# Optimization experiments

Hardware: AMD Instinct MI355X
Metric: run time of the kernel (lower is better)

The kernel has to match this reference:

```python
import jax, jax.numpy as jnp
import numpy as np

EPS = float(np.finfo(np.float32).eps)
B, N, NUM_ATOM, K = 16, 256, 64, 20
NUM_EDGETYPE = 3
SHORT = (1, 2, 3)
LONG = (3, 5, 7)
HIDDEN = (128, 128)
OUT = 1
SCALES = len(SHORT) + len(LONG) + NUM_EDGETYPE + 1  # 10
LB = 1e-4  # lanczos breakdown tolerance


def _xavier(k, fi, fo):
    return jax.random.uniform(k, (fi, fo), jnp.float32, -1.0, 1.0) * (6.0 / (fi + fo)) ** 0.5


def setup_inputs() -> dict:
    key = jax.random.key(0)
    ks = jax.random.split(key, 12)
    inp = {}
    inp["node_feat"] = jax.random.randint(ks[0], (B, N), 0, NUM_ATOM)
    inp["L"] = jax.random.uniform(ks[1], (B, N, N, NUM_EDGETYPE + 1), jnp.float32)
    # embedding_map: Linear(num_atom,1024) -> ReLU -> Linear(1024,num_atom)
    inp["emb_w1"] = _xavier(ks[2], NUM_ATOM, 1024); inp["emb_b1"] = jnp.zeros((1024,), jnp.float32)
    inp["emb_w2"] = _xavier(ks[3], 1024, NUM_ATOM); inp["emb_b2"] = jnp.zeros((NUM_ATOM,), jnp.float32)
    # eigen_map per long scale: Linear(K*K,1024) -> ReLU -> Linear(1024,K*K)
    S, K2 = len(LONG), K * K
    inp["eig_w1"] = jnp.stack([_xavier(jax.random.fold_in(ks[4], i), K2, 1024) for i in range(S)])
    inp["eig_b1"] = jnp.zeros((S, 1024), jnp.float32)
    inp["eig_w2"] = jnp.stack([_xavier(jax.random.fold_in(ks[5], i), 1024, K2) for i in range(S)])
    inp["eig_b2"] = jnp.zeros((S, K2), jnp.float32)
    dims = [NUM_ATOM] + list(HIDDEN) + [OUT]
    inp["filt_w0"] = _xavier(ks[6], dims[0] * SCALES, dims[1]); inp["filt_b0"] = jnp.zeros((dims[1],), jnp.float32)
    inp["filt_w1"] = _xavier(ks[7], dims[1] * SCALES, dims[2]); inp["filt_b1"] = jnp.zeros((dims[2],), jnp.float32)
    inp["filt_wo"] = _xavier(ks[8], dims[2], dims[3]); inp["filt_bo"] = jnp.zeros((dims[3],), jnp.float32)
    inp["att_w"] = _xavier(ks[9], dims[2], 1); inp["att_b"] = jnp.zeros((1,), jnp.float32)
    return inp


def _graph_laplacian(feat, adj_mask):
    # feat: B x N x D; pairwise gaussian affinity, sym-normalized (alpha=0.5)
    diff = feat[:, :, None, :] - feat[:, None, :, :]           # B,N,N,D
    dist2 = jnp.sum(diff * diff, axis=-1).reshape(B, -1)       # B,N*N
    sigma2 = jnp.mean(dist2, axis=1, keepdims=True)
    A = jnp.exp(-dist2 / sigma2).reshape(B, N, N) * adj_mask
    row_sum = jnp.sum(A, axis=2, keepdims=True)
    pad = jnp.where(row_sum == 0.0, 1.0, 0.0)
    D = 1.0 / jnp.sqrt(row_sum + pad)
    return D * A * jnp.swapaxes(D, 1, 2)


def _lanczos(A, key):
    # sequential Lanczos tridiagonalization with double Gram-Schmidt reorth
    q = jax.random.normal(key, (B, N), jnp.float32)
    q = q / jnp.linalg.norm(q, axis=1, keepdims=True)

    def step(carry, i):
        Qbuf, q_prev, qc, beta_prev, valid = carry
        z = jnp.einsum('bij,bj->bi', A, qc)
        alpha = jnp.sum(qc * z, axis=1)
        z = z - alpha[:, None] * qc - beta_prev[:, None] * q_prev
        for _ in range(2):  # reorthogonalize against Q[1..ii-1] (zero cols are no-ops)
            coef = jnp.einsum('bnk,bn->bk', Qbuf, z) / (jnp.sum(Qbuf * Qbuf, axis=1) + EPS)
            z = z - jnp.einsum('bnk,bk->bn', Qbuf, coef)
        beta = jnp.sqrt(jnp.sum(z * z, axis=1))
        valid = valid * (beta >= LB).astype(jnp.float32)
        q_next = z * valid[:, None] / (beta[:, None] + EPS)
        Qbuf = Qbuf.at[:, :, i].set(qc)
        return (Qbuf, qc, q_next, beta, valid), (alpha, beta, valid, qc)

    init = (jnp.zeros((B, N, K), jnp.float32), jnp.zeros((B, N), jnp.float32), q,
            jnp.zeros((B,), jnp.float32), jnp.ones((B,), jnp.float32))
    _, (alphas, betas, valids, qs) = jax.lax.scan(step, init, jnp.arange(K))
    alpha = alphas.T            # B,K
    beta = betas.T              # B,K
    valid = valids.T            # B,K (cumulative 1..1 0..0)
    idx = jnp.sum(valid, axis=1).astype(jnp.int32)   # rank per sample
    alpha = alpha * valid
    beta = beta[:, :K - 1] * valid[:, :K - 1]
    T = jax.vmap(lambda a, b: jnp.diag(a) + jnp.diag(b, 1) + jnp.diag(b, -1))(alpha, beta)
    Q = jnp.transpose(qs, (1, 2, 0))  # B,N,K
    # faithful to source: zero node rows >= idx_mask (only when idx < N)
    row_ok = (jnp.arange(N)[None, :] < idx[:, None]) | (idx[:, None] >= N)
    Q = Q * valid[:, None, :] * row_ok[:, :, None].astype(jnp.float32)
    return T, Q


def _spectral_filters(T, Q, eig_w1, eig_b1, eig_w2, eig_b2, key):
    T_list = []
    TT = T
    b = jax.random.normal(key, (B, K, 1), jnp.float32)
    Tb = b / jnp.linalg.norm(b, axis=1, keepdims=True)
    for ii in range(max(LONG) + 1):
        if ii in LONG:
            T_list.append(TT)
        TT = TT @ T
        # power-iteration cap on spectral radius
        Tb_new = T @ Tb
        l_max = jnp.sum(Tb_new * Tb, axis=1, keepdims=True) / (jnp.sum(Tb * Tb, axis=1, keepdims=True) + EPS)
        TT = TT * (jnp.abs(l_max) <= 1.0).astype(jnp.float32)
        Tb = Tb_new / (jnp.linalg.norm(Tb_new, axis=1, keepdims=True) + EPS)
    triu = jnp.triu(jnp.ones((K, K), jnp.float32))
    eye = jnp.eye(K, dtype=jnp.float32)
    outs = []
    for s in range(len(LONG)):
        h = jax.nn.relu(T_list[s].reshape(B, -1) @ eig_w1[s] + eig_b1[s])
        DD = (h @ eig_w2[s] + eig_b2[s]).reshape(B, K, K)
        DD = DD * triu
        DD = DD + jnp.swapaxes(DD, 1, 2) * (1.0 - eye)  # symmetrize
        outs.append(jnp.einsum('bnk,bkl,bml->bnm', Q, DD, Q))
    return jnp.stack(outs, axis=3)  # B,N,N,S


def reference(node_feat, L, emb_w1, emb_b1, emb_w2, emb_b2, eig_w1, eig_b1, eig_w2, eig_b2,
              filt_w0, filt_b0, filt_w1, filt_b1, filt_wo, filt_bo, att_w, att_b):
    key = jax.random.key(42)
    state = jax.nn.one_hot(node_feat, NUM_ATOM, dtype=jnp.float32)  # frozen identity embedding
    feat = jax.nn.relu(state @ emb_w1 + emb_b1) @ emb_w2 + emb_b2
    Lk = _graph_laplacian(feat, L[:, :, :, 0])
    T, Q = _lanczos(Lk, jax.random.fold_in(key, 0))
    filt_w = (filt_w0, filt_w1)
    filt_b = (filt_b0, filt_b1)
    for tt in range(len(HIDDEN)):
        msg = []
        DD = _spectral_filters(T, Q, eig_w1, eig_b1, eig_w2, eig_b2, jax.random.fold_in(key, tt + 1))
        tmp = state
        for ii in range(1, max(SHORT) + 1):  # short diffusion
            tmp = jnp.einsum('bij,bjd->bid', Lk, tmp)
            if ii in SHORT:
                msg.append(tmp)
        for s in range(len(LONG)):           # long (spectral) diffusion
            msg.append(jnp.einsum('bij,bjd->bid', DD[:, :, :, s], state))
        for e in range(NUM_EDGETYPE + 1):     # per-edgetype propagation
            msg.append(jnp.einsum('bij,bjd->bid', L[:, :, :, e], state))
        msg = jnp.concatenate(msg, axis=2)    # B,N,10*D
        state = jax.nn.relu(msg @ filt_w[tt] + filt_b[tt])
    y = state @ filt_wo + filt_bo             # B,N,1
    att = jax.nn.sigmoid(state @ att_w + att_b)
    score = jnp.mean(att * y, axis=1)          # B,OUT (mask=None -> mean over nodes)
    return score
```

## Files before the change

kernel.cpp:

```cpp
#include <hip/hip_runtime.h>


constexpr int nB = 16;
constexpr int nN = 256;
constexpr int nK = 20;
constexpr int QS = nN + 1;
constexpr float EPSF = 1.1920928955078125e-07f;
constexpr float LBF  = 1e-4f;

#define DEV static __device__ __forceinline__

DEV void tf2x32(unsigned k0, unsigned k1, unsigned x0, unsigned x1,
                unsigned &o0, unsigned &o1) {
  unsigned ks2 = k0 ^ k1 ^ 0x1BD11BDAu;
#define RND(r) { x0 += x1; x1 = (x1 << r) | (x1 >> (32 - r)); x1 ^= x0; }
  x0 += k0;  x1 += k1;
  RND(13) RND(15) RND(26) RND(6)
  x0 += k1;  x1 += ks2 + 1u;
  RND(17) RND(29) RND(16) RND(24)
  x0 += ks2; x1 += k0 + 2u;
  RND(13) RND(15) RND(26) RND(6)
  x0 += k0;  x1 += k1 + 3u;
  RND(17) RND(29) RND(16) RND(24)
  x0 += k1;  x1 += ks2 + 4u;
  RND(13) RND(15) RND(26) RND(6)
  x0 += ks2; x1 += k0 + 5u;
#undef RND
  o0 = x0; o1 = x1;
}

DEV float erfinv_f32(float x) {
  float w = -log1pf(-x * x);
  float p;
  if (w < 5.0f) {
    w -= 2.5f;
    p = 2.81022636e-08f;
    p = fmaf(p, w, 3.43273939e-07f);
    p = fmaf(p, w, -3.5233877e-06f);
    p = fmaf(p, w, -4.39150654e-06f);
    p = fmaf(p, w, 0.00021858087f);
    p = fmaf(p, w, -0.00125372503f);
    p = fmaf(p, w, -0.00417768164f);
    p = fmaf(p, w, 0.246640727f);
    p = fmaf(p, w, 1.50140941f);
  } else {
    w = sqrtf(w) - 3.0f;
    p = -0.000200214257f;
    p = fmaf(p, w, 0.000100950558f);
    p = fmaf(p, w, 0.00134934322f);
    p = fmaf(p, w, -0.00367342844f);
    p = fmaf(p, w, 0.00573950773f);
    p = fmaf(p, w, -0.0076224613f);
    p = fmaf(p, w, 0.00943887047f);
    p = fmaf(p, w, 1.00167406f);
    p = fmaf(p, w, 2.83297682f);
  }
  return p * x;
}

DEV float jax_normal(unsigned k0, unsigned k1, unsigned idx) {
  unsigned o0, o1;
  tf2x32(k0, k1, 0u , idx , o0, o1);
  unsigned bits = o0 ^ o1;
  float u = __uint_as_float((bits >> 9) | 0x3f800000u) - 1.0f;
  const float lo = -0.99999994f;
  float v = fmaxf(lo, u * 2.0f + lo);
  return 1.41421356237309515f * erfinv_f32(v);
}

DEV double waveRedD(double v) {
#pragma unroll
  for (int m = 32; m > 0; m >>= 1) v += __shfl_xor(v, m, 64);
  return v;
}
DEV float waveRedF(float v) {
#pragma unroll
  for (int m = 32; m > 0; m >>= 1) v += __shfl_xor(v, m, 64);
  return v;
}
DEV double blockSumD(double v, double *s4) {
  v = waveRedD(v);
  int w = threadIdx.x >> 6;
  __syncthreads();
  if ((threadIdx.x & 63) == 0) s4[w] = v;
  __syncthreads();
  return s4[0] + s4[1] + s4[2] + s4[3];
}
DEV double sum8(const double *r) {
  return ((r[0] + r[1]) + (r[2] + r[3])) + ((r[4] + r[5]) + (r[6] + r[7]));
}

__global__ __launch_bounds__(256) void feat_table_kernel(
    const float *__restrict__ w1, const float *__restrict__ b1,
    const float *__restrict__ w2, const float *__restrict__ b2,
    float *__restrict__ table) {
  int a = blockIdx.x, t = threadIdx.x;
  __shared__ float hh[1024];
  __shared__ float part[256];
  for (int k = t; k < 1024; k += 256)
    hh[k] = fmaxf(w1[(size_t)a * 1024 + k] + b1[k], 0.f);
  __syncthreads();
  int d = t & 63, slice = t >> 6;
  float acc = 0.f;
  for (int k = slice * 256; k < slice * 256 + 256; k++)
    acc += hh[k] * w2[(size_t)k * 64 + d];
  part[t] = acc;
  __syncthreads();
  if (t < 64)
    table[(size_t)a * 64 + t] =
        part[t] + part[64 + t] + part[128 + t] + part[192 + t] + b2[t];
}

__global__ __launch_bounds__(256) void feat_state_tr_kernel(
    const int *__restrict__ nf, const float *__restrict__ table,
    float *__restrict__ feat, float *__restrict__ featT,
    float *__restrict__ state0) {
  int g = blockIdx.x;
  int bb = g >> 2, n0 = (g & 3) * 64;
  int t = threadIdx.x;
  int c = t & 63, r4 = t >> 6;
  __shared__ float tl[64][65];
  __shared__ int av[64];
  if (t < 64) av[t] = nf[bb * nN + n0 + t];
  __syncthreads();
  for (int r = r4; r < 64; r += 4) {
    int a = av[r];
    float v = table[(size_t)a * 64 + c];
    tl[r][c] = v;
    feat[((size_t)(bb * nN + n0 + r)) * 64 + c] = v;
    state0[((size_t)(bb * nN + n0 + r)) * 64 + c] = (c == a) ? 1.f : 0.f;
  }
  __syncthreads();
  for (int r = r4; r < 64; r += 4)
    featT[(size_t)bb * 16384 + (size_t)r * nN + n0 + c] = tl[c][r];
}

__global__ __launch_bounds__(256) void dist2_kernel(
    const float *__restrict__ feat, const float *__restrict__ featT,
    float *__restrict__ G, double *__restrict__ part) {
  int g = blockIdx.x;
  int bb = g >> 6, i0 = (g & 63) * 4;
  int t = threadIdx.x;
  __shared__ float fi[4][64];
  __shared__ double s4[4];
  {
    int r = t >> 6, d = t & 63;
    fi[r][d] = feat[((size_t)(bb * nN + i0 + r)) * 64 + d];
  }
  __syncthreads();
  const float *ft = featT + (size_t)bb * 16384 + t;
  float a0 = 0.f, a1 = 0.f, a2 = 0.f, a3 = 0.f;
#pragma unroll 8
  for (int d = 0; d < 64; d++) {
    float x = ft[(size_t)d * nN];
    float d0 = fi[0][d] - x; a0 += d0 * d0;
    float d1 = fi[1][d] - x; a1 += d1 * d1;
    float d2 = fi[2][d] - x; a2 += d2 * d2;
    float d3 = fi[3][d] - x; a3 += d3 * d3;
  }
  size_t base = ((size_t)bb * nN + i0) * nN + t;
  G[base]           = a0;
  G[base + nN]      = a1;
  G[base + 2 * nN]  = a2;
  G[base + 3 * nN]  = a3;
  double tot = blockSumD((double)a0 + (double)a1 + (double)a2 + (double)a3, s4);
  if (t == 0) part[g] = tot;
}

__global__ __launch_bounds__(64) void sigred_kernel(
    const double *__restrict__ part, float *__restrict__ sigma2) {
  int bb = blockIdx.x, t = threadIdx.x;
  double v = part[(size_t)bb * 64 + t];
  v = waveRedD(v);
  if (t == 0) sigma2[bb] = (float)(v / 65536.0);
}

__global__ __launch_bounds__(256) void arow_kernel(
    const float *__restrict__ Lfull, const float *__restrict__ sigma2,
    float *__restrict__ G, float *__restrict__ Dv) {
  int g = blockIdx.x;
  int i = g % nN, bb = g / nN;
  int t = threadIdx.x;
  __shared__ double s4[4];
  float sig = sigma2[bb];
  size_t idx2 = ((size_t)bb * nN + i) * nN + t;
  float a = expf(-G[idx2] / sig) * Lfull[idx2 * 4];
  G[idx2] = a;
  double rs = blockSumD((double)a, s4);
  if (t == 0) {
    float r = (float)rs;
    float pad = (r == 0.f) ? 1.f : 0.f;
    Dv[(size_t)bb * nN + i] = 1.f / sqrtf(r + pad);
  }
}

__global__ __launch_bounds__(256) void lkscale_tr_kernel(
    float *__restrict__ G, const float *__restrict__ Dv,
    float *__restrict__ GT) {
  int g = blockIdx.x;
  int bb = g >> 4, tile = g & 15;
  int ti = (tile >> 2) * 64, tj = (tile & 3) * 64;
  int t = threadIdx.x;
  int lj = t & 63, li0 = t >> 6;
  __shared__ float tl[64][65];
  for (int r = li0; r < 64; r += 4) {
    int i = ti + r;
    size_t idx = ((size_t)bb * nN + i) * nN + tj + lj;
    float v = Dv[(size_t)bb * nN + i] * G[idx] * Dv[(size_t)bb * nN + tj + lj];
    G[idx] = v;
    tl[r][lj] = v;
  }
  __syncthreads();
  for (int r = li0; r < 64; r += 4) {
    int j = tj + r;
    GT[((size_t)bb * nN + j) * nN + ti + lj] = tl[lj][r];
  }
}

__global__ __launch_bounds__(512)
void lanczos_kernel(const float *__restrict__ GT, float *__restrict__ Qout,
                    float *__restrict__ Tout) {
  __shared__ float Qb[nK * QS];
  __shared__ float qc[nN], qp[nN], zz[nN];
  __shared__ double zp[2][nN];
  __shared__ float qn2[nK], sAl[nK], sBe[nK], sVa[nK], coef[nK];
  __shared__ double redA[8], redB[8];
  int bb = blockIdx.x, u = threadIdx.x;
  int t = u & 255, h = u >> 8;
  int wv = u >> 6, lane = u & 63;
  int gid = u >> 4, gl = u & 15;

  const float *Gcol = GT + (size_t)bb * (nN * nN) + (size_t)(h * 128) * nN + t;

  unsigned k0, k1;
  tf2x32(0u, 42u, 0u, 0u, k0, k1);
  float val = 0.f;
  if (h == 0) val = jax_normal(k0, k1, (unsigned)(bb * nN + t));
  {
    double v = waveRedD((double)val * (double)val);
    __syncthreads();
    if (lane == 0) redA[wv] = v;
    __syncthreads();
    double n2 = sum8(redA);
    if (h == 0) {
      qc[t] = val / sqrtf((float)n2);
      qp[t] = 0.f;
    }
  }
  __syncthreads();

  float beta_prev = 0.f, validf = 1.f;

  for (int i = 0; i < nK; i++) {
    double a0 = 0, a1 = 0, a2 = 0, a3 = 0, a4 = 0, a5 = 0, a6 = 0, a7 = 0;
    {
      const float *qv = qc + h * 128;
#pragma unroll
      for (int jj = 0; jj < 128; jj += 8) {
        a0 += (double)Gcol[(size_t)(jj + 0) * nN] * (double)qv[jj + 0];
        a1 += (double)Gcol[(size_t)(jj + 1) * nN] * (double)qv[jj + 1];
        a2 += (double)Gcol[(size_t)(jj + 2) * nN] * (double)qv[jj + 2];
        a3 += (double)Gcol[(size_t)(jj + 3) * nN] * (double)qv[jj + 3];
        a4 += (double)Gcol[(size_t)(jj + 4) * nN] * (double)qv[jj + 4];
        a5 += (double)Gcol[(size_t)(jj + 5) * nN] * (double)qv[jj + 5];
        a6 += (double)Gcol[(size_t)(jj + 6) * nN] * (double)qv[jj + 6];
        a7 += (double)Gcol[(size_t)(jj + 7) * nN] * (double)qv[jj + 7];
      }
    }
    double part = ((a0 + a1) + (a2 + a3)) + ((a4 + a5) + (a6 + a7));
    zp[h][t] = part;
    double apart = (double)qc[t] * part;
    double qpart = (h == 0) ? (double)qc[t] * (double)qc[t] : 0.0;
    apart = waveRedD(apart);
    qpart = waveRedD(qpart);
    if (lane == 0) { redA[wv] = apart; redB[wv] = qpart; }
    __syncthreads();
    float alpha = (float)sum8(redA);
    if (h == 0) {
      float zi = (float)(zp[0][t] + zp[1][t]);
      zi = zi - alpha * qc[t] - beta_prev * qp[t];
      zz[t] = zi;
    } else {
      Qb[i * QS + t] = qc[t];
      if (t == 0) qn2[i] = (float)sum8(redB);
    }
    __syncthreads();
    if (gid < i) {
      double p = 0.0;
#pragma unroll
      for (int j = 0; j < 16; j++) {
        int n0 = gl + 16 * j;
        p += (double)Qb[gid * QS + n0] * (double)zz[n0];
      }
#pragma unroll
      for (int m = 1; m <= 8; m <<= 1) p += __shfl_xor(p, m, 64);
      if (gl == 0)
        coef[gid] = (float)(p / ((double)qn2[gid] + (double)EPSF));
    }
    __syncthreads();
    if (h == 0) {
      double sub = 0.0;
      for (int k = 0; k < i; k++)
        sub += (double)Qb[k * QS + t] * (double)coef[k];
      zz[t] = (float)((double)zz[t] - sub);
    }
    __syncthreads();
    if (gid < i) {
      double p = 0.0;
#pragma unroll
      for (int j = 0; j < 16; j++) {
        int n0 = gl + 16 * j;
        p += (double)Qb[gid * QS + n0] * (double)zz[n0];
      }
#pragma unroll
      for (int m = 1; m <= 8; m <<= 1) p += __shfl_xor(p, m, 64);
      if (gl == 0)
        coef[gid] = (float)(p / ((double)qn2[gid] + (double)EPSF));
    }
    __syncthreads();
    double bpart = 0.0;
    if (h == 0) {
      double sub = 0.0;
      for (int k = 0; k < i; k++)
        sub += (double)Qb[k * QS + t] * (double)coef[k];
      float znew = (float)((double)zz[t] - sub);
      zz[t] = znew;
      bpart = (double)znew * (double)znew;
    }
    bpart = waveRedD(bpart);
    if (lane == 0) redA[wv] = bpart;
    __syncthreads();
    float beta = sqrtf((float)sum8(redA));
    validf *= (beta >= LBF) ? 1.f : 0.f;
    if (u == 0) {
      sAl[i] = alpha;
      sBe[i] = beta;
      sVa[i] = validf;
    }
    if (h == 0) {
      float qnext = zz[t] * validf / (beta + EPSF);
      qp[t] = qc[t];
      qc[t] = qnext;
    }
    __syncthreads();
    beta_prev = beta;
  }

  float idxf = 0.f;
  for (int k = 0; k < nK; k++) idxf += sVa[k];
  int idx = (int)idxf;
  if (h == 0) {
    float rowok = ((t < idx) || (idx >= nN)) ? 1.f : 0.f;
    for (int k = 0; k < nK; k++)
      Qout[((size_t)bb * nN + t) * nK + k] = Qb[k * QS + t] * sVa[k] * rowok;
  }
  for (int e = u; e < nK * nK; e += 512) {
    int i = e / nK, j = e % nK;
    float v = 0.f;
    if (i == j) v = sAl[i] * sVa[i];
    else if (j == i + 1) v = sBe[i] * sVa[i];
    else if (i == j + 1) v = sBe[j] * sVa[j];
    Tout[(size_t)bb * nK * nK + e] = v;
  }
}

__global__ __launch_bounds__(64) void spect_power_kernel(
    const float *__restrict__ Tin, float *__restrict__ Tpow2) {
  __shared__ float T_[nK * nK], TT[nK * nK], TTn[nK * nK];
  __shared__ float Tb[nK], Tbn[nK];
  int bb = blockIdx.x & 15, tt = blockIdx.x >> 4;
  int t = threadIdx.x;
  for (int e = t; e < nK * nK; e += 64) {
    float v = Tin[(size_t)bb * nK * nK + e];
    T_[e] = v;
    TT[e] = v;
  }
  unsigned k0, k1;
  tf2x32(0u, 42u, 0u, (unsigned)(tt + 1), k0, k1);
  if (t < nK) Tb[t] = jax_normal(k0, k1, (unsigned)(bb * nK + t));
  __syncthreads();
  float pv = (t < nK) ? Tb[t] * Tb[t] : 0.f;
  float nb = sqrtf(waveRedF(pv));
  if (t < nK) Tb[t] = Tb[t] / nb;
  __syncthreads();
  for (int ii = 0; ii < 8; ii++) {
    if (ii == 3 || ii == 5 || ii == 7) {
      int s = (ii - 3) / 2;
      int sf = tt * 3 + s;
      for (int e = t; e < nK * nK; e += 64)
        Tpow2[((size_t)sf * nB + bb) * nK * nK + e] = TT[e];
    }
    __syncthreads();
    for (int e = t; e < nK * nK; e += 64) {
      int i = e / nK, j = e % nK;
      float a = 0.f;
      for (int l = 0; l < nK; l++) a += TT[i * nK + l] * T_[l * nK + j];
      TTn[e] = a;
    }
    if (t < nK) {
      float a = 0.f;
      for (int l = 0; l < nK; l++) a += T_[t * nK + l] * Tb[l];
      Tbn[t] = a;
    }
    __syncthreads();
    float pn = (t < nK) ? Tbn[t] * Tb[t] : 0.f;
    float pd = (t < nK) ? Tb[t] * Tb[t] : 0.f;
    float num = waveRedF(pn);
    float den = waveRedF(pd);
    float lmax = num / (den + EPSF);
    float keep = (fabsf(lmax) <= 1.0f) ? 1.f : 0.f;
    __syncthreads();
    for (int e = t; e < nK * nK; e += 64) TT[e] = TTn[e] * keep;
    float p2 = (t < nK) ? Tbn[t] * Tbn[t] : 0.f;
    float nn = sqrtf(waveRedF(p2));
    if (t < nK) Tb[t] = Tbn[t] / (nn + EPSF);
    __syncthreads();
  }
}

__global__ __launch_bounds__(256) void eig1_kernel(
    const float *__restrict__ Tpow2, const float *__restrict__ w1p,
    const float *__restrict__ b1p, float *__restrict__ h2) {
  int g = blockIdx.x;
  int oc = g & 15, sf = g >> 4;
  int sw = sf % 3;
  int t = threadIdx.x;
  int o = (t & 63) + oc * 64, bbg = t >> 6;
  __shared__ float tp[nB * 400];
  for (int e = t; e < nB * 400; e += 256)
    tp[e] = Tpow2[(size_t)sf * nB * 400 + e];
  __syncthreads();
  float bias = b1p[(size_t)sw * 1024 + o];
  float acc0 = bias, acc1 = bias, acc2 = bias, acc3 = bias;
  const float *W = w1p + (size_t)sw * 400 * 1024 + o;
  const float *t0 = tp + (bbg + 0) * 400;
  const float *t1 = tp + (bbg + 4) * 400;
  const float *t2 = tp + (bbg + 8) * 400;
  const float *t3 = tp + (bbg + 12) * 400;
  for (int k = 0; k < 400; k++) {
    float w = W[(size_t)k * 1024];
    acc0 += t0[k] * w;
    acc1 += t1[k] * w;
    acc2 += t2[k] * w;
    acc3 += t3[k] * w;
  }
  h2[((size_t)sf * nB + (bbg + 0))  * 1024 + o] = fmaxf(acc0, 0.f);
  h2[((size_t)sf * nB + (bbg + 4))  * 1024 + o] = fmaxf(acc1, 0.f);
  h2[((size_t)sf * nB + (bbg + 8))  * 1024 + o] = fmaxf(acc2, 0.f);
  h2[((size_t)sf * nB + (bbg + 12)) * 1024 + o] = fmaxf(acc3, 0.f);
}

__global__ __launch_bounds__(256) void eig2_kernel(
    const float *__restrict__ h2, const float *__restrict__ w2p,
    const float *__restrict__ b2p, float *__restrict__ raw2) {
  int g = blockIdx.x;
  int kc = g % 25, sf = g / 25;
  int sw = sf % 3;
  int t = threadIdx.x;
  int kl = (t & 15) + kc * 16, bb = t >> 4;
  __shared__ float hh[nB * 1025];
  for (int e = t; e < nB * 1024; e += 256)
    hh[(e >> 10) * 1025 + (e & 1023)] = h2[(size_t)sf * nB * 1024 + e];
  __syncthreads();
  float acc = b2p[(size_t)sw * 400 + kl];
  const float *W = w2p + (size_t)sw * 1024 * 400 + kl;
  const float *hv = hh + bb * 1025;
  for (int o = 0; o < 1024; o++) acc += hv[o] * W[(size_t)o * 400];
  raw2[((size_t)sf * nB + bb) * 400 + kl] = acc;
}

__global__ void qtstate_kernel(const float *__restrict__ Q,
                               const float *__restrict__ state,
                               float *__restrict__ E) {
  int g = blockIdx.x;
  int k = g % nK, bb = g / nK;
  int t = threadIdx.x, Din = blockDim.x;
  __shared__ float qcol[nN];
  for (int n = t; n < nN; n += Din) qcol[n] = Q[((size_t)bb * nN + n) * nK + k];
  __syncthreads();
  const float *st = state + (size_t)bb * nN * Din;
  float acc = 0.f;
  for (int n = 0; n < nN; n++) acc += qcol[n] * st[(size_t)n * Din + t];
  E[((size_t)bb * nK + k) * Din + t] = acc;
}

__global__ void ddE_kernel(const float *__restrict__ raw,
                           const float *__restrict__ E,
                           float *__restrict__ F) {
  int g = blockIdx.x;
  int k = g % nK, bb = (g / nK) % nB, s = g / (nK * nB);
  int t = threadIdx.x, Din = blockDim.x;
  __shared__ float dr[nK];
  if (t < nK) {
    int mi = k < t ? k : t, ma = k < t ? t : k;
    dr[t] = raw[((size_t)s * nB + bb) * 400 + mi * nK + ma];
  }
  __syncthreads();
  float acc = 0.f;
  for (int l = 0; l < nK; l++)
    acc += dr[l] * E[((size_t)bb * nK + l) * Din + t];
  F[(((size_t)s * nB + bb) * nK + k) * Din + t] = acc;
}

__global__ void lk_matvec_kernel(const float *__restrict__ Lk,
                                 const float *__restrict__ in, int inStride,
                                 float *__restrict__ out, int outStride) {
  int g = blockIdx.x;
  int bb = g >> 5, r0 = (g & 31) * 8;
  int t = threadIdx.x, Din = blockDim.x;
  __shared__ float rows[8][nN];
  for (int e = t; e < 8 * nN; e += Din) {
    int r = e >> 8, j = e & 255;
    rows[r][j] = Lk[((size_t)bb * nN + r0 + r) * nN + j];
  }
  __syncthreads();
  float acc[8] = {0.f, 0.f, 0.f, 0.f, 0.f, 0.f, 0.f, 0.f};
  const float *ip = in + (size_t)bb * nN * inStride + t;
  for (int j = 0; j < nN; j++) {
    float x = ip[(size_t)j * inStride];
#pragma unroll
    for (int r = 0; r < 8; r++) acc[r] += rows[r][j] * x;
  }
#pragma unroll
  for (int r = 0; r < 8; r++)
    out[((size_t)bb * nN + r0 + r) * outStride + t] = acc[r];
}

__global__ void longmsg_kernel(const float *__restrict__ Q,
                               const float *__restrict__ F,
                               float *__restrict__ msg, int C) {
  int g = blockIdx.x;
  int i = g % nN, bb = g / nN;
  int t = threadIdx.x, Din = blockDim.x;
  __shared__ float qr[nK];
  if (t < nK) qr[t] = Q[((size_t)bb * nN + i) * nK + t];
  __syncthreads();
  for (int s = 0; s < 3; s++) {
    float acc = 0.f;
    for (int k = 0; k < nK; k++)
      acc += qr[k] * F[(((size_t)s * nB + bb) * nK + k) * Din + t];
    msg[((size_t)bb * nN + i) * C + (3 + s) * Din + t] = acc;
  }
}

__global__ void edgemsg_kernel(const float *__restrict__ Lfull,
                               const float *__restrict__ state,
                               float *__restrict__ msg, int C) {
  int g = blockIdx.x;
  int bb = g >> 6, r0 = (g & 63) * 4;
  int t = threadIdx.x, Din = blockDim.x;
  __shared__ float4 rows4[4][nN];
  const float4 *L4 = (const float4 *)Lfull;
  for (int e = t; e < 4 * nN; e += Din) {
    int r = e >> 8, j = e & 255;
    rows4[r][j] = L4[((size_t)bb * nN + r0 + r) * nN + j];
  }
  __syncthreads();
  float acc[4][4];
#pragma unroll
  for (int r = 0; r < 4; r++)
#pragma unroll
    for (int e = 0; e < 4; e++) acc[r][e] = 0.f;
  const float *st = state + (size_t)bb * nN * Din + t;
  for (int j = 0; j < nN; j++) {
    float x = st[(size_t)j * Din];
#pragma unroll
    for (int r = 0; r < 4; r++) {
      float4 lv = rows4[r][j];
      acc[r][0] += lv.x * x;
      acc[r][1] += lv.y * x;
      acc[r][2] += lv.z * x;
      acc[r][3] += lv.w * x;
    }
  }
#pragma unroll
  for (int r = 0; r < 4; r++)
#pragma unroll
    for (int e = 0; e < 4; e++)
      msg[((size_t)bb * nN + r0 + r) * C + (6 + e) * Din + t] = acc[r][e];
}

__global__ __launch_bounds__(256) void filt_kernel(
    const float *__restrict__ msg, const float *__restrict__ W,
    const float *__restrict__ bias, float *__restrict__ out, int C) {
  int g = blockIdx.x;
  int base = g * 16;
  int t = threadIdx.x;
  int o = t & 127, ih = t >> 7;
  __shared__ float mt[16][64];
  __shared__ float wt[64][128];
  float acc[8];
  float bo = bias[o];
#pragma unroll
  for (int r = 0; r < 8; r++) acc[r] = bo;
  for (int c0 = 0; c0 < C; c0 += 64) {
    __syncthreads();
    for (int e = t; e < 16 * 64; e += 256) {
      int r = e >> 6, c = e & 63;
      mt[r][c] = msg[((size_t)(base + r)) * C + c0 + c];
    }
    for (int e = t; e < 64 * 128; e += 256)
      wt[e >> 7][e & 127] = W[(size_t)(c0 + (e >> 7)) * 128 + (e & 127)];
    __syncthreads();
    for (int c = 0; c < 64; c++) {
      float w = wt[c][o];
#pragma unroll
      for (int r = 0; r < 8; r++) acc[r] += mt[ih * 8 + r][c] * w;
    }
  }
#pragma unroll
  for (int r = 0; r < 8; r++)
    out[((size_t)(base + ih * 8 + r)) * 128 + o] = fmaxf(acc[r], 0.f);
}

__global__ __launch_bounds__(256) void score_kernel(
    const float *__restrict__ state, const float *__restrict__ wo,
    const float *__restrict__ bo, const float *__restrict__ aw,
    const float *__restrict__ ab, float *__restrict__ out) {
  __shared__ float sl[64 * 129];
  __shared__ double s4[4];
  int bb = blockIdx.x, t = threadIdx.x;
  float bof = bo[0], abf = ab[0];
  double dsum = 0.0;
  for (int r0 = 0; r0 < nN; r0 += 64) {
    __syncthreads();
    for (int e = t; e < 64 * 128; e += 256) {
      int r = e >> 7, o = e & 127;
      sl[r * 129 + o] = state[((size_t)bb * nN + r0 + r) * 128 + o];
    }
    __syncthreads();
    if (t < 64) {
      const float *sr = sl + t * 129;
      float sy = bof, sa = abf;
      for (int o = 0; o < 128; o++) {
        float v = sr[o];
        sy += v * wo[o];
        sa += v * aw[o];
      }
      float att = 1.f / (1.f + expf(-sa));
      dsum += (double)(att * sy);
    }
  }
  double m = blockSumD(dsum, s4);
  if (t == 0) out[bb] = (float)(m / (double)nN);
}

extern "C" void kernel_launch(void *const *d_in, const int *in_sizes, int n_in,
                              void *d_out, int out_size, void *d_ws,
                              size_t ws_size, hipStream_t stream) {
  (void)in_sizes; (void)n_in; (void)out_size;
  const int   *node_feat = (const int *)d_in[0];
  const float *Lfull     = (const float *)d_in[1];
  const float *emb_w1    = (const float *)d_in[2];
  const float *emb_b1    = (const float *)d_in[3];
  const float *emb_w2    = (const float *)d_in[4];
  const float *emb_b2    = (const float *)d_in[5];
  const float *eig_w1    = (const float *)d_in[6];
  const float *eig_b1    = (const float *)d_in[7];
  const float *eig_w2    = (const float *)d_in[8];
  const float *eig_b2    = (const float *)d_in[9];
  const float *filt_w0   = (const float *)d_in[10];
  const float *filt_b0   = (const float *)d_in[11];
  const float *filt_w1   = (const float *)d_in[12];
  const float *filt_b1   = (const float *)d_in[13];
  const float *filt_wo   = (const float *)d_in[14];
  const float *filt_bo   = (const float *)d_in[15];
  const float *att_w     = (const float *)d_in[16];
  const float *att_b     = (const float *)d_in[17];

  float *ws   = (float *)d_ws;
  float *G    = ws;
  float *msg  = G + 1048576;
  float *st0  = msg + 5242880;
  float *st1  = st0 + 262144;
  float *st2  = st1 + 524288;
  float *feat = st2 + 524288;
  float *table= feat + 262144;
  float *Q    = table + 4096;
  float *T    = Q + 81920;
  float *Tpow = T + 6400;
  float *DD   = Tpow + 19200;
  float *h    = DD + 19200;
  float *E    = h + 49152;
  float *F    = E + 40960;
  float *Dv   = F + 122880;
  double *part   = (double *)(Dv + 4096);
  float  *sigma2 = (float *)(part + nB * nN);
  float *GT    = msg;
  float *featT = msg + 1048576;
  float *Tpow2 = feat;
  float *raw2  = feat + 38400;
  float *h2    = feat + 76800;
  const size_t needBytes = (size_t)(8220432) * 4;
  if (ws_size < needBytes) return;

  feat_table_kernel<<<64, 256, 0, stream>>>(emb_w1, emb_b1, emb_w2, emb_b2, table);
  feat_state_tr_kernel<<<nB * 4, 256, 0, stream>>>(node_feat, table, feat,
                                                   featT, st0);
  dist2_kernel<<<nB * 64, 256, 0, stream>>>(feat, featT, G, part);
  sigred_kernel<<<nB, 64, 0, stream>>>(part, sigma2);
  arow_kernel<<<nB * nN, 256, 0, stream>>>(Lfull, sigma2, G, Dv);
  lkscale_tr_kernel<<<nB * 16, 256, 0, stream>>>(G, Dv, GT);
  lanczos_kernel<<<nB, 512, 0, stream>>>(GT, Q, T);
  spect_power_kernel<<<nB * 2, 64, 0, stream>>>(T, Tpow2);
  eig1_kernel<<<96, 256, 0, stream>>>(Tpow2, eig_w1, eig_b1, h2);
  eig2_kernel<<<150, 256, 0, stream>>>(h2, eig_w2, eig_b2, raw2);

  const float *stateIn = st0;
  float *stOut[2] = {st1, st2};
  int Din = 64;
  for (int tt = 0; tt < 2; tt++) {
    int C = 10 * Din;
    const float *rawT = raw2 + (size_t)tt * 3 * nB * 400;
    qtstate_kernel<<<nB * nK, Din, 0, stream>>>(Q, stateIn, E);
    ddE_kernel<<<3 * nB * nK, Din, 0, stream>>>(rawT, E, F);
    lk_matvec_kernel<<<nB * nN / 8, Din, 0, stream>>>(G, stateIn, Din, msg + 0 * Din, C);
    lk_matvec_kernel<<<nB * nN / 8, Din, 0, stream>>>(G, msg + 0 * Din, C, msg + 1 * Din, C);
    lk_matvec_kernel<<<nB * nN / 8, Din, 0, stream>>>(G, msg + 1 * Din, C, msg + 2 * Din, C);
    longmsg_kernel<<<nB * nN, Din, 0, stream>>>(Q, F, msg, C);
    edgemsg_kernel<<<nB * nN / 4, Din, 0, stream>>>(Lfull, stateIn, msg, C);
    filt_kernel<<<nB * nN / 16, 256, 0, stream>>>(
        msg, tt ? filt_w1 : filt_w0, tt ? filt_b1 : filt_b0, stOut[tt], C);
    stateIn = stOut[tt];
    Din = 128;
  }
  score_kernel<<<nB, 256, 0, stream>>>(st2, filt_wo, filt_bo, att_w, att_b,
                                       (float *)d_out);
}
```

Measured before the change: 742.8 us.

## Merge independent message kernels into three heterogeneous launches by dependency level

```diff
diff --git a/kernel.cpp b/kernel.cpp
--- a/kernel.cpp
+++ b/kernel.cpp
@@ -469,115 +469,164 @@
   raw2[((size_t)sf * nB + bb) * 400 + kl] = acc;
 }
 
-__global__ void qtstate_kernel(const float *__restrict__ Q,
-                               const float *__restrict__ state,
-                               float *__restrict__ E) {
-  int g = blockIdx.x;
-  int k = g % nK, bb = g / nK;
+__global__ void msgD1_kernel(const float *__restrict__ Q,
+                             const float *__restrict__ state,
+                             float *__restrict__ E,
+                             const float *__restrict__ Lk,
+                             float *__restrict__ msg,
+                             const float *__restrict__ Lfull, int C) {
+  __shared__ __align__(16) char smem[16384];
   int t = threadIdx.x, Din = blockDim.x;
-  __shared__ float qcol[nN];
-  for (int n = t; n < nN; n += Din) qcol[n] = Q[((size_t)bb * nN + n) * nK + k];
-  __syncthreads();
-  const float *st = state + (size_t)bb * nN * Din;
-  float acc = 0.f;
-  for (int n = 0; n < nN; n++) acc += qcol[n] * st[(size_t)n * Din + t];
-  E[((size_t)bb * nK + k) * Din + t] = acc;
-}
-
-__global__ void ddE_kernel(const float *__restrict__ raw,
-                           const float *__restrict__ E,
-                           float *__restrict__ F) {
-  int g = blockIdx.x;
-  int k = g % nK, bb = (g / nK) % nB, s = g / (nK * nB);
+  int gb = blockIdx.x;
+  if (gb < nB * nK) {
+    int k = gb % nK, bb = gb / nK;
+    float *qcol = (float *)smem;
+    for (int n = t; n < nN; n += Din)
+      qcol[n] = Q[((size_t)bb * nN + n) * nK + k];
+    __syncthreads();
+    const float *st = state + (size_t)bb * nN * Din;
+    float acc = 0.f;
+    for (int n = 0; n < nN; n++) acc += qcol[n] * st[(size_t)n * Din + t];
+    E[((size_t)bb * nK + k) * Din + t] = acc;
+  } else if (gb < nB * nK + nB * nN / 8) {
+    int g = gb - nB * nK;
+    int bb = g >> 5, r0 = (g & 31) * 8;
+    float (*rows)[nN] = (float (*)[nN])smem;
+    for (int e = t; e < 8 * nN; e += Din) {
+      int r = e >> 8, j = e & 255;
+      rows[r][j] = Lk[((size_t)bb * nN + r0 + r) * nN + j];
+    }
+    __syncthreads();
+    float acc[8] = {0.f, 0.f, 0.f, 0.f, 0.f, 0.f, 0.f, 0.f};
+    const float *ip = state + (size_t)bb * nN * Din + t;
+    for (int j = 0; j < nN; j++) {
+      float x = ip[(size_t)j * Din];
+#pragma unroll
+      for (int r = 0; r < 8; r++) acc[r] += rows[r][j] * x;
+    }
+#pragma unroll
+    for (int r = 0; r < 8; r++)
+      out_store: ;
+#pragma unroll
+    for (int r = 0; r < 8; r++)
+      msg[((size_t)bb * nN + r0 + r) * C + 0 * Din + t] = acc[r];
+  } else {
+    int g = gb - nB * nK - nB * nN / 8;
+    int bb = g >> 6, r0 = (g & 63) * 4;
+    float4 (*rows4)[nN] = (float4 (*)[nN])smem;
+    const float4 *L4 = (const float4 *)Lfull;
+    for (int e = t; e < 4 * nN; e += Din) {
+      int r = e >> 8, j = e & 255;
+      rows4[r][j] = L4[((size_t)bb * nN + r0 + r) * nN + j];
+    }
+    __syncthreads();
+    float acc[4][4];
+#pragma unroll
+    for (int r = 0; r < 4; r++)
+#pragma unroll
+      for (int e = 0; e < 4; e++) acc[r][e] = 0.f;
+    const float *st = state + (size_t)bb * nN * Din + t;
+    for (int j = 0; j < nN; j++) {
+      float x = st[(size_t)j * Din];
+#pragma unroll
+      for (int r = 0; r < 4; r++) {
+        float4 lv = rows4[r][j];
+        acc[r][0] += lv.x * x;
+        acc[r][1] += lv.y * x;
+        acc[r][2] += lv.z * x;
+        acc[r][3] += lv.w * x;
+      }
+    }
+#pragma unroll
+    for (int r = 0; r < 4; r++)
+#pragma unroll
+      for (int e = 0; e < 4; e++)
+        msg[((size_t)bb * nN + r0 + r) * C + (6 + e) * Din + t] = acc[r][e];
+  }
+}
+
+__global__ void msgD2_kernel(const float *__restrict__ raw,
+                             const float *__restrict__ E,
+                             float *__restrict__ F,
+                             const float *__restrict__ Lk,
+                             float *__restrict__ msg, int C) {
+  __shared__ __align__(16) char smem[8192];
   int t = threadIdx.x, Din = blockDim.x;
-  __shared__ float dr[nK];
-  if (t < nK) {
-    int mi = k < t ? k : t, ma = k < t ? t : k;
-    dr[t] = raw[((size_t)s * nB + bb) * 400 + mi * nK + ma];
-  }
-  __syncthreads();
-  float acc = 0.f;
-  for (int l = 0; l < nK; l++)
-    acc += dr[l] * E[((size_t)bb * nK + l) * Din + t];
-  F[(((size_t)s * nB + bb) * nK + k) * Din + t] = acc;
-}
-
-__global__ void lk_matvec_kernel(const float *__restrict__ Lk,
-                                 const float *__restrict__ in, int inStride,
-                                 float *__restrict__ out, int outStride) {
-  int g = blockIdx.x;
-  int bb = g >> 5, r0 = (g & 31) * 8;
+  int gb = blockIdx.x;
+  if (gb < 3 * nB * nK) {
+    int g = gb;
+    int k = g % nK, bb = (g / nK) % nB, s = g / (nK * nB);
+    float *dr = (float *)smem;
+    if (t < nK) {
+      int mi = k < t ? k : t, ma = k < t ? t : k;
+      dr[t] = raw[((size_t)s * nB + bb) * 400 + mi * nK + ma];
+    }
+    __syncthreads();
+    float acc = 0.f;
+    for (int l = 0; l < nK; l++)
+      acc += dr[l] * E[((size_t)bb * nK + l) * Din + t];
+    F[(((size_t)s * nB + bb) * nK + k) * Din + t] = acc;
+  } else {
+    int g = gb - 3 * nB * nK;
+    int bb = g >> 5, r0 = (g & 31) * 8;
+    float (*rows)[nN] = (float (*)[nN])smem;
+    for (int e = t; e < 8 * nN; e += Din) {
+      int r = e >> 8, j = e & 255;
+      rows[r][j] = Lk[((size_t)bb * nN + r0 + r) * nN + j];
+    }
+    __syncthreads();
+    float acc[8] = {0.f, 0.f, 0.f, 0.f, 0.f, 0.f, 0.f, 0.f};
+    const float *ip = msg + (size_t)bb * nN * C + 0 * Din + t;
+    for (int j = 0; j < nN; j++) {
+      float x = ip[(size_t)j * C];
+#pragma unroll
+      for (int r = 0; r < 8; r++) acc[r] += rows[r][j] * x;
+    }
+#pragma unroll
+    for (int r = 0; r < 8; r++)
+      msg[((size_t)bb * nN + r0 + r) * C + 1 * Din + t] = acc[r];
+  }
+}
+
+__global__ void msgD3_kernel(const float *__restrict__ Q,
+                             const float *__restrict__ F,
+                             const float *__restrict__ Lk,
+                             float *__restrict__ msg, int C) {
+  __shared__ __align__(16) char smem[8192];
   int t = threadIdx.x, Din = blockDim.x;
-  __shared__ float rows[8][nN];
-  for (int e = t; e < 8 * nN; e += Din) {
-    int r = e >> 8, j = e & 255;
-    rows[r][j] = Lk[((size_t)bb * nN + r0 + r) * nN + j];
-  }
-  __syncthreads();
-  float acc[8] = {0.f, 0.f, 0.f, 0.f, 0.f, 0.f, 0.f, 0.f};
-  const float *ip = in + (size_t)bb * nN * inStride + t;
-  for (int j = 0; j < nN; j++) {
-    float x = ip[(size_t)j * inStride];
-#pragma unroll
-    for (int r = 0; r < 8; r++) acc[r] += rows[r][j] * x;
-  }
-#pragma unroll
-  for (int r = 0; r < 8; r++)
-    out[((size_t)bb * nN + r0 + r) * outStride + t] = acc[r];
-}
-
-__global__ void longmsg_kernel(const float *__restrict__ Q,
-                               const float *__restrict__ F,
-                               float *__restrict__ msg, int C) {
-  int g = blockIdx.x;
-  int i = g % nN, bb = g / nN;
-  int t = threadIdx.x, Din = blockDim.x;
-  __shared__ float qr[nK];
-  if (t < nK) qr[t] = Q[((size_t)bb * nN + i) * nK + t];
-  __syncthreads();
-  for (int s = 0; s < 3; s++) {
-    float acc = 0.f;
-    for (int k = 0; k < nK; k++)
-      acc += qr[k] * F[(((size_t)s * nB + bb) * nK + k) * Din + t];
-    msg[((size_t)bb * nN + i) * C + (3 + s) * Din + t] = acc;
-  }
-}
-
-__global__ void edgemsg_kernel(const float *__restrict__ Lfull,
-                               const float *__restrict__ state,
-                               float *__restrict__ msg, int C) {
-  int g = blockIdx.x;
-  int bb = g >> 6, r0 = (g & 63) * 4;
-  int t = threadIdx.x, Din = blockDim.x;
-  __shared__ float4 rows4[4][nN];
-  const float4 *L4 = (const float4 *)Lfull;
-  for (int e = t; e < 4 * nN; e += Din) {
-    int r = e >> 8, j = e & 255;
-    rows4[r][j] = L4[((size_t)bb * nN + r0 + r) * nN + j];
-  }
-  __syncthreads();
-  float acc[4][4];
-#pragma unroll
-  for (int r = 0; r < 4; r++)
-#pragma unroll
-    for (int e = 0; e < 4; e++) acc[r][e] = 0.f;
-  const float *st = state + (size_t)bb * nN * Din + t;
-  for (int j = 0; j < nN; j++) {
-    float x = st[(size_t)j * Din];
-#pragma unroll
-    for (int r = 0; r < 4; r++) {
-      float4 lv = rows4[r][j];
-      acc[r][0] += lv.x * x;
-      acc[r][1] += lv.y * x;
-      acc[r][2] += lv.z * x;
-      acc[r][3] += lv.w * x;
-    }
-  }
-#pragma unroll
-  for (int r = 0; r < 4; r++)
-#pragma unroll
-    for (int e = 0; e < 4; e++)
-      msg[((size_t)bb * nN + r0 + r) * C + (6 + e) * Din + t] = acc[r][e];
+  int gb = blockIdx.x;
+  if (gb < nB * nN) {
+    int g = gb;
+    int i = g % nN, bb = g / nN;
+    float *qr = (float *)smem;
+    if (t < nK) qr[t] = Q[((size_t)bb * nN + i) * nK + t];
+    __syncthreads();
+    for (int s = 0; s < 3; s++) {
+      float acc = 0.f;
+      for (int k = 0; k < nK; k++)
+        acc += qr[k] * F[(((size_t)s * nB + bb) * nK + k) * Din + t];
+      msg[((size_t)bb * nN + i) * C + (3 + s) * Din + t] = acc;
+    }
+  } else {
+    int g = gb - nB * nN;
+    int bb = g >> 5, r0 = (g & 31) * 8;
+    float (*rows)[nN] = (float (*)[nN])smem;
+    for (int e = t; e < 8 * nN; e += Din) {
+      int r = e >> 8, j = e & 255;
+      rows[r][j] = Lk[((size_t)bb * nN + r0 + r) * nN + j];
+    }
+    __syncthreads();
+    float acc[8] = {0.f, 0.f, 0.f, 0.f, 0.f, 0.f, 0.f, 0.f};
+    const float *ip = msg + (size_t)bb * nN * C + 1 * Din + t;
+    for (int j = 0; j < nN; j++) {
+      float x = ip[(size_t)j * C];
+#pragma unroll
+      for (int r = 0; r < 8; r++) acc[r] += rows[r][j] * x;
+    }
+#pragma unroll
+    for (int r = 0; r < 8; r++)
+      msg[((size_t)bb * nN + r0 + r) * C + 2 * Din + t] = acc[r];
+  }
 }
 
 __global__ __launch_bounds__(256) void filt_kernel(
@@ -709,16 +758,18 @@
   const float *stateIn = st0;
   float *stOut[2] = {st1, st2};
   int Din = 64;
+  const int QTB = nB * nK;
+  const int LKB = nB * nN / 8;
+  const int EDB = nB * nN / 4;
+  const int DDB = 3 * nB * nK;
+  const int LMB = nB * nN;
   for (int tt = 0; tt < 2; tt++) {
     int C = 10 * Din;
     const float *rawT = raw2 + (size_t)tt * 3 * nB * 400;
-    qtstate_kernel<<<nB * nK, Din, 0, stream>>>(Q, stateIn, E);
-    ddE_kernel<<<3 * nB * nK, Din, 0, stream>>>(rawT, E, F);
-    lk_matvec_kernel<<<nB * nN / 8, Din, 0, stream>>>(G, stateIn, Din, msg + 0 * Din, C);
-    lk_matvec_kernel<<<nB * nN / 8, Din, 0, stream>>>(G, msg + 0 * Din, C, msg + 1 * Din, C);
-    lk_matvec_kernel<<<nB * nN / 8, Din, 0, stream>>>(G, msg + 1 * Din, C, msg + 2 * Din, C);
-    longmsg_kernel<<<nB * nN, Din, 0, stream>>>(Q, F, msg, C);
-    edgemsg_kernel<<<nB * nN / 4, Din, 0, stream>>>(Lfull, stateIn, msg, C);
+    msgD1_kernel<<<QTB + LKB + EDB, Din, 0, stream>>>(Q, stateIn, E, G, msg,
+                                                      Lfull, C);
+    msgD2_kernel<<<DDB + LKB, Din, 0, stream>>>(rawT, E, F, G, msg, C);
+    msgD3_kernel<<<LMB + LKB, Din, 0, stream>>>(Q, F, G, msg, C);
     filt_kernel<<<nB * nN / 16, 256, 0, stream>>>(
         msg, tt ? filt_w1 : filt_w0, tt ? filt_b1 : filt_b0, stOut[tt], C);
     stateIn = stOut[tt];
```

Result: faster. 660.1 us (-11.1%).
